# Performance work log

Hardware: AMD Instinct MI355X
Metric: run time of the kernel (lower is better)

## Reference

```python
import jax, jax.numpy as jnp
import numpy as np

B, T, C = 2, 2048, 1024
H = 16
D = C // H  # 64
SCALE = 1.0 / np.sqrt(D)


def setup_inputs() -> dict:
    key = jax.random.key(0)
    k1, k2, k3 = jax.random.split(key, 3)
    x = jax.random.normal(k1, (B, T, C), dtype=jnp.float32)
    Wqkv = jax.random.normal(k2, (C, 3 * C), dtype=jnp.float32) * 0.02
    bqkv = jnp.zeros((3 * C,), dtype=jnp.float32)
    Wo = jax.random.normal(k3, (C, C), dtype=jnp.float32) * 0.02
    bo = jnp.zeros((C,), dtype=jnp.float32)
    return {"x": x, "Wqkv": Wqkv, "bqkv": bqkv, "Wo": Wo, "bo": bo}


def reference(x, Wqkv, bqkv, Wo, bo):
    Bsz, Tlen, Cdim = x.shape
    qkv = x @ Wqkv + bqkv                       # [B,T,3C]
    qkv = qkv.reshape(Bsz, Tlen, 3, H, D)
    qkv = jnp.transpose(qkv, (2, 0, 3, 1, 4))   # [3,B,H,T,D]
    q, k, v = qkv[0], qkv[1], qkv[2]
    att = jnp.einsum("bhqd,bhkd->bhqk", q, k) * SCALE
    # NOTE: faithful to source: mask keeps positions where k >= q
    i = jnp.arange(Tlen)
    mask = i[None, :] >= i[:, None]             # [T,T], entry [q,k]: k >= q
    att = jnp.where(mask[None, None], att, -jnp.inf)
    att = jax.nn.softmax(att, axis=-1)
    # dropout p=0.0 (inference) -> identity
    y = jnp.einsum("bhqk,bhkd->bhqd", att, v)   # [B,H,T,D]
    y = jnp.transpose(y, (0, 2, 1, 3)).reshape(Bsz, Tlen, Cdim)
    y = y @ Wo + bo
    return y
```

## Files before the change

kernel.cpp:

```cpp
#include <hip/hip_runtime.h>
#include <hip/hip_bf16.h>
#include <cstdint>
#include <cstddef>

typedef __bf16 bf16_t;
typedef __bf16 bf16x8 __attribute__((ext_vector_type(8)));
typedef __bf16 bf16x4 __attribute__((ext_vector_type(4)));
typedef short short4v __attribute__((ext_vector_type(4)));
typedef float f32x4 __attribute__((ext_vector_type(4)));

#define NB 2
#define NT 2048
#define NC 1024
#define NH 16
#define ND 64
#define NM (NB * NT)
#define N3 (3 * NC)
#define QSCALE_LOG2E 0.18033688011112042f

#define GLOAD_LDS16(gptr, lptr)                                                          \
  __builtin_amdgcn_global_load_lds((const __attribute__((address_space(1))) void*)(gptr), \
                                   (__attribute__((address_space(3))) void*)(lptr), 16, 0, 0)

__global__ __launch_bounds__(256) void cast_f32_bf16_k(const float* __restrict__ in,
                                                       bf16_t* __restrict__ out, int n) {
  int i = (blockIdx.x * 256 + threadIdx.x) * 4;
  if (i + 3 < n) {
    const float4 v = *(const float4*)(in + i);
    bf16x4 o;
    o[0] = (bf16_t)v.x; o[1] = (bf16_t)v.y; o[2] = (bf16_t)v.z; o[3] = (bf16_t)v.w;
    *(bf16x4*)(out + i) = o;
  }
}

__global__ __launch_bounds__(256) void transpose_cast_k(const float* __restrict__ in,
                                                        bf16_t* __restrict__ out,
                                                        int R, int Ccols) {
  __shared__ float tile[32][33];
  int tc = blockIdx.x * 32;
  int tr = blockIdx.y * 32;
  int lx = threadIdx.x & 31;
  int ly = threadIdx.x >> 5;
#pragma unroll
  for (int i = 0; i < 32; i += 8)
    tile[ly + i][lx] = in[(size_t)(tr + ly + i) * Ccols + tc + lx];
  __syncthreads();
#pragma unroll
  for (int i = 0; i < 32; i += 8)
    out[(size_t)(tc + ly + i) * R + tr + lx] = (bf16_t)tile[lx][ly + i];
}

template <int K>
__device__ __forceinline__ void gemm_mainloop(const bf16_t* __restrict__ A,
                                              const bf16_t* __restrict__ Bt,
                                              int m0, int n0, f32x4 acc[4][4],
                                              bf16_t* lds) {
  bf16_t* As = lds;
  bf16_t* Bs = lds + 4096;
  const int tid = threadIdx.x;
  const int lane = tid & 63;
  const int w = tid >> 6;
  const int wm = (w & 1) * 64;
  const int wn = (w >> 1) * 64;
  const int quad = lane >> 4;
  const int l16 = lane & 15;

  for (int k0 = 0; k0 < K; k0 += 32) {
#pragma unroll
    for (int i = 0; i < 2; ++i) {
      const int gb = w * 128 + i * 64;
      const int g = gb + lane;
      GLOAD_LDS16(A + (size_t)(m0 + (g >> 2)) * K + k0 + (g & 3) * 8, As + gb * 8);
      GLOAD_LDS16(Bt + (size_t)(n0 + (g >> 2)) * K + k0 + (g & 3) * 8, Bs + gb * 8);
    }
    __syncthreads();
    bf16x8 af[4], bfr[4];
#pragma unroll
    for (int i = 0; i < 4; ++i)
      af[i] = *(const bf16x8*)(As + (wm + i * 16 + l16) * 32 + quad * 8);
#pragma unroll
    for (int j = 0; j < 4; ++j)
      bfr[j] = *(const bf16x8*)(Bs + (wn + j * 16 + l16) * 32 + quad * 8);
#pragma unroll
    for (int i = 0; i < 4; ++i)
#pragma unroll
      for (int j = 0; j < 4; ++j)
        acc[i][j] = __builtin_amdgcn_mfma_f32_16x16x32_bf16(af[i], bfr[j], acc[i][j], 0, 0, 0);
    __syncthreads();
  }
}

__global__ __launch_bounds__(256) void qkv_gemm_k(const bf16_t* __restrict__ A,
                                                  const bf16_t* __restrict__ Bt,
                                                  const float* __restrict__ bias,
                                                  bf16_t* __restrict__ qb,
                                                  bf16_t* __restrict__ kb,
                                                  bf16_t* __restrict__ vb) {
  __shared__ __align__(16) bf16_t lds[8192];
  const int m0 = blockIdx.y * 128, n0 = blockIdx.x * 128;
  f32x4 acc[4][4] = {};
  gemm_mainloop<NC>(A, Bt, m0, n0, acc, lds);

  const int lane = threadIdx.x & 63;
  const int w = threadIdx.x >> 6;
  const int wm = (w & 1) * 64, wn = (w >> 1) * 64;
  const int quad = lane >> 4, l16 = lane & 15;
#pragma unroll
  for (int i = 0; i < 4; ++i)
#pragma unroll
    for (int j = 0; j < 4; ++j) {
      const int n = n0 + wn + j * 16 + l16;
      const float bn = bias[n];
      const int which = n >> 10;
      const int rem = n & 1023;
      const int h = rem >> 6, d = rem & 63;
      bf16_t* dst = (which == 0) ? qb : (which == 1) ? kb : vb;
      const float sc = (which == 0) ? QSCALE_LOG2E : 1.0f;
#pragma unroll
      for (int r = 0; r < 4; ++r) {
        const int m = m0 + wm + i * 16 + quad * 4 + r;
        const int b = m >> 11, t = m & 2047;
        const size_t bh = (size_t)b * NH + h;
        dst[(bh * NT + t) * ND + d] = (bf16_t)((acc[i][j][r] + bn) * sc);
      }
    }
}

__global__ __launch_bounds__(256) void vtile_k(const bf16_t* __restrict__ v,
                                               bf16_t* __restrict__ vt2) {
  const int bh = blockIdx.x >> 5, c = blockIdx.x & 31;
  const bf16_t* src = v + ((size_t)bh * NT + c * 64) * ND;
  bf16_t* dst = vt2 + ((size_t)bh * 32 + c) * 4096;
#pragma unroll
  for (int it = 0; it < 4; ++it) {
    const int slot = it * 256 + threadIdx.x;
    const int g = slot >> 6, d = slot & 63;
    bf16x4 val;
#pragma unroll
    for (int j = 0; j < 4; ++j) val[j] = src[(size_t)(g * 4 + j) * ND + d];
    *(bf16x4*)(dst + (size_t)slot * 4) = val;
  }
}

__global__ __launch_bounds__(256, 4) void attn_k(const bf16_t* __restrict__ q,
                                                 const bf16_t* __restrict__ k,
                                                 const bf16_t* __restrict__ vt2,
                                                 bf16_t* __restrict__ y ) {
  const int bh = blockIdx.x & 31;
  const int u = (blockIdx.x >> 5) & 7;
  const int r4 = blockIdx.x >> 8;
  const int T = r4 * 8 + ((r4 & 1) ? (7 - u) : u);
  const int b = bh >> 4, h = bh & 15;

  const bf16_t* qp = q + (size_t)bh * NT * ND;
  const bf16_t* kp = k + (size_t)bh * NT * ND;
  const bf16_t* vp = vt2 + (size_t)bh * 32 * 4096;

  __shared__ __align__(16) bf16_t kbuf[2][4096];
  __shared__ __align__(16) bf16_t vbuf[2][4096];

  const int lane = threadIdx.x & 63;
  const int w = threadIdx.x >> 6;
  const int quad = lane >> 4, l16 = lane & 15;
  const int qv = T * 64 + w * 16 + l16;

  const bf16x8 qf0 = *(const bf16x8*)(qp + (size_t)qv * ND + quad * 8);
  const bf16x8 qf1 = *(const bf16x8*)(qp + (size_t)qv * ND + 32 + quad * 8);

  float m = -INFINITY, l = 0.f;
  f32x4 o[4];
#pragma unroll
  for (int dj = 0; dj < 4; ++dj) o[dj] = (f32x4){0.f, 0.f, 0.f, 0.f};

  auto stage = [&](int c, int bi) {
    const bf16_t* kc = kp + (size_t)c * 64 * ND;
    const bf16_t* vc = vp + (size_t)c * 4096;
#pragma unroll
    for (int i = 0; i < 2; ++i) {
      const int gb = w * 128 + i * 64;
      const int s = gb + lane;
      const int row = s >> 3;
      const int cs = (s & 7) ^ (row & 7);
      GLOAD_LDS16(kc + ((size_t)row * 8 + cs) * 8, kbuf[bi] + gb * 8);
      GLOAD_LDS16(vc + (size_t)s * 8, vbuf[bi] + gb * 8);
    }
  };

  stage(T, 0);
  int cur = 0;
  for (int c = T; c < 32; ++c) {
    __syncthreads();
    if (c + 1 < 32) stage(c + 1, cur ^ 1);

    const bf16_t* kt = kbuf[cur];
    const bf16_t* vt = vbuf[cur];
    const int t0 = c * 64;

    f32x4 sv[4];
#pragma unroll
    for (int kj = 0; kj < 4; ++kj) {
      const int kr = kj * 16 + l16;
      const int sw = kr & 7;
      const bf16x8 a0 = *(const bf16x8*)(kt + ((size_t)kr * 8 + (quad ^ sw)) * 8);
      const bf16x8 a1 = *(const bf16x8*)(kt + ((size_t)kr * 8 + ((4 + quad) ^ sw)) * 8);
      f32x4 z = {0.f, 0.f, 0.f, 0.f};
      z = __builtin_amdgcn_mfma_f32_16x16x32_bf16(a0, qf0, z, 0, 0, 0);
      z = __builtin_amdgcn_mfma_f32_16x16x32_bf16(a1, qf1, z, 0, 0, 0);
      sv[kj] = z;
    }
    if (c == T) {
#pragma unroll
      for (int kj = 0; kj < 4; ++kj)
#pragma unroll
        for (int r = 0; r < 4; ++r)
          if (t0 + kj * 16 + quad * 4 + r < qv) sv[kj][r] = -INFINITY;
    }
    float mx = -INFINITY;
#pragma unroll
    for (int kj = 0; kj < 4; ++kj)
#pragma unroll
      for (int r = 0; r < 4; ++r) mx = fmaxf(mx, sv[kj][r]);
    mx = fmaxf(mx, __shfl_xor(mx, 16));
    mx = fmaxf(mx, __shfl_xor(mx, 32));
    const float mnew = fmaxf(m, mx);
    const float alpha = exp2f(m - mnew);
    m = mnew;
    float rs = 0.f;
#pragma unroll
    for (int kj = 0; kj < 4; ++kj)
#pragma unroll
      for (int r = 0; r < 4; ++r) {
        const float p = exp2f(sv[kj][r] - mnew);
        sv[kj][r] = p;
        rs += p;
      }
    rs += __shfl_xor(rs, 16);
    rs += __shfl_xor(rs, 32);
    l = l * alpha + rs;
    short4v pf[4];
#pragma unroll
    for (int kj = 0; kj < 4; ++kj) {
      bf16x4 pb;
#pragma unroll
      for (int r = 0; r < 4; ++r) pb[r] = (bf16_t)sv[kj][r];
      pf[kj] = __builtin_bit_cast(short4v, pb);
    }
#pragma unroll
    for (int dj = 0; dj < 4; ++dj) {
      o[dj][0] *= alpha; o[dj][1] *= alpha; o[dj][2] *= alpha; o[dj][3] *= alpha;
#pragma unroll
      for (int kj = 0; kj < 4; ++kj) {
        const bf16x4 a =
            *(const bf16x4*)(vt + ((size_t)(kj * 4 + quad) * 64 + dj * 16 + l16) * 4);
        o[dj] = __builtin_amdgcn_mfma_f32_16x16x16bf16_1k(
            __builtin_bit_cast(short4v, a), pf[kj], o[dj], 0, 0, 0);
      }
    }
    cur ^= 1;
  }

  const float inv = 1.0f / l;
  const size_t base = ((size_t)b * NT + qv) * NC + h * 64;
#pragma unroll
  for (int dj = 0; dj < 4; ++dj) {
    bf16x4 va;
#pragma unroll
    for (int r = 0; r < 4; ++r) va[r] = (bf16_t)(o[dj][r] * inv);
    *(bf16x4*)(y + base + dj * 16 + quad * 4) = va;
  }
}

__global__ __launch_bounds__(256) void out_gemm_k(const bf16_t* __restrict__ A,
                                                  const bf16_t* __restrict__ Bt,
                                                  const float* __restrict__ bias,
                                                  float* __restrict__ out) {
  __shared__ __align__(16) bf16_t lds[8192];
  const int m0 = blockIdx.y * 128, n0 = blockIdx.x * 128;
  f32x4 acc[4][4] = {};
  gemm_mainloop<NC>(A, Bt, m0, n0, acc, lds);

  const int lane = threadIdx.x & 63;
  const int w = threadIdx.x >> 6;
  const int wm = (w & 1) * 64, wn = (w >> 1) * 64;
  const int quad = lane >> 4, l16 = lane & 15;
#pragma unroll
  for (int i = 0; i < 4; ++i)
#pragma unroll
    for (int j = 0; j < 4; ++j) {
      const int n = n0 + wn + j * 16 + l16;
      const float bn = bias[n];
#pragma unroll
      for (int r = 0; r < 4; ++r) {
        const int m = m0 + wm + i * 16 + quad * 4 + r;
        out[(size_t)m * NC + n] = acc[i][j][r] + bn;
      }
    }
}

extern "C" void kernel_launch(void* const* d_in, const int* in_sizes, int n_in,
                              void* d_out, int out_size, void* d_ws, size_t ws_size,
                              hipStream_t stream) {
  const float* x = (const float*)d_in[0];
  const float* Wqkv = (const float*)d_in[1];
  const float* bqkv = (const float*)d_in[2];
  const float* Wo = (const float*)d_in[3];
  const float* bo = (const float*)d_in[4];
  float* out = (float*)d_out;

  char* p = (char*)d_ws;
  bf16_t* xbf = (bf16_t*)p;   p += (size_t)NM * NC * sizeof(bf16_t);
  bf16_t* wqkvT = (bf16_t*)p; p += (size_t)N3 * NC * sizeof(bf16_t);
  bf16_t* woT = (bf16_t*)p;   p += (size_t)NC * NC * sizeof(bf16_t);
  bf16_t* qb = (bf16_t*)p;    p += (size_t)NB * NH * NT * ND * sizeof(bf16_t);
  bf16_t* kb = (bf16_t*)p;    p += (size_t)NB * NH * NT * ND * sizeof(bf16_t);
  bf16_t* vb = (bf16_t*)p;    p += (size_t)NB * NH * NT * ND * sizeof(bf16_t);
  bf16_t* yb = (bf16_t*)p;    p += (size_t)NM * NC * sizeof(bf16_t);
  bf16_t* vt2 = xbf;

  hipLaunchKernelGGL(cast_f32_bf16_k, dim3(NM * NC / 1024), dim3(256), 0, stream,
                     x, xbf, NM * NC);
  hipLaunchKernelGGL(transpose_cast_k, dim3(N3 / 32, NC / 32), dim3(256), 0, stream,
                     Wqkv, wqkvT, NC, N3);
  hipLaunchKernelGGL(transpose_cast_k, dim3(NC / 32, NC / 32), dim3(256), 0, stream,
                     Wo, woT, NC, NC);
  hipLaunchKernelGGL(qkv_gemm_k, dim3(N3 / 128, NM / 128), dim3(256), 0, stream,
                     xbf, wqkvT, bqkv, qb, kb, vb);
  hipLaunchKernelGGL(vtile_k, dim3(32 * 32), dim3(256), 0, stream, vb, vt2);
  hipLaunchKernelGGL(attn_k, dim3(1024), dim3(256), 0, stream, qb, kb, vt2, yb);
  hipLaunchKernelGGL(out_gemm_k, dim3(NC / 128, NM / 128), dim3(256), 0, stream,
                     yb, woT, bo, out);
}
```

Baseline: 194.6 us.

## Fuse prep kernels, write V tiled from QKV GEMM, MFMA rowsum in attention

The x cast and both weight transpose-casts are merged into one prep launch. The QKV GEMM epilogue now writes V directly in the tiled layout attention expects, which removes the separate vtile kernel and its extra pass over memory. In attention, the softmax row sum is computed with an MFMA against a ones vector from the bf16-rounded probabilities instead of a scalar reduction with shuffles. The rescale of the output accumulator is skipped when no lane's max changed. Together these aim to cut launch overhead, memory traffic and VALU work. The cost is a warp-wide vote per tile and a row sum taken from bf16-rounded values.

```diff
diff --git a/kernel.cpp b/kernel.cpp
--- a/kernel.cpp
+++ b/kernel.cpp
@@ -22,32 +22,39 @@
   __builtin_amdgcn_global_load_lds((const __attribute__((address_space(1))) void*)(gptr), \
                                    (__attribute__((address_space(3))) void*)(lptr), 16, 0, 0)
 
-__global__ __launch_bounds__(256) void cast_f32_bf16_k(const float* __restrict__ in,
-                                                       bf16_t* __restrict__ out, int n) {
-  int i = (blockIdx.x * 256 + threadIdx.x) * 4;
-  if (i + 3 < n) {
-    const float4 v = *(const float4*)(in + i);
+__global__ __launch_bounds__(256) void prep_k(const float* __restrict__ x,
+                                              const float* __restrict__ Wqkv,
+                                              const float* __restrict__ Wo,
+                                              bf16_t* __restrict__ xbf,
+                                              bf16_t* __restrict__ wqkvT,
+                                              bf16_t* __restrict__ woT) {
+  __shared__ float tile[32][33];
+  const int bx = blockIdx.x;
+  if (bx < 4096) {
+    const int i = (bx * 256 + threadIdx.x) * 4;
+    const float4 v = *(const float4*)(x + i);
     bf16x4 o;
     o[0] = (bf16_t)v.x; o[1] = (bf16_t)v.y; o[2] = (bf16_t)v.z; o[3] = (bf16_t)v.w;
-    *(bf16x4*)(out + i) = o;
+    *(bf16x4*)(xbf + i) = o;
+    return;
   }
-}
-
-__global__ __launch_bounds__(256) void transpose_cast_k(const float* __restrict__ in,
-                                                        bf16_t* __restrict__ out,
-                                                        int R, int Ccols) {
-  __shared__ float tile[32][33];
-  int tc = blockIdx.x * 32;
-  int tr = blockIdx.y * 32;
-  int lx = threadIdx.x & 31;
-  int ly = threadIdx.x >> 5;
+  const int t = bx - 4096;
+  const int cxi = t & 127;
+  const int tr = (t >> 7) * 32;
+  const float* in;
+  bf16_t* out;
+  int Ccols, tc;
+  if (cxi < 96) { in = Wqkv; out = wqkvT; Ccols = 3072; tc = cxi * 32; }
+  else          { in = Wo;   out = woT;   Ccols = 1024; tc = (cxi - 96) * 32; }
+  const int lx = threadIdx.x & 31;
+  const int ly = threadIdx.x >> 5;
 #pragma unroll
   for (int i = 0; i < 32; i += 8)
     tile[ly + i][lx] = in[(size_t)(tr + ly + i) * Ccols + tc + lx];
   __syncthreads();
 #pragma unroll
   for (int i = 0; i < 32; i += 8)
-    out[(size_t)(tc + ly + i) * R + tr + lx] = (bf16_t)tile[lx][ly + i];
+    out[(size_t)(tc + ly + i) * 1024 + tr + lx] = (bf16_t)tile[lx][ly + i];
 }
 
 template <int K>
@@ -95,7 +102,7 @@
                                                   const float* __restrict__ bias,
                                                   bf16_t* __restrict__ qb,
                                                   bf16_t* __restrict__ kb,
-                                                  bf16_t* __restrict__ vb) {
+                                                  bf16_t* __restrict__ vt2) {
   __shared__ __align__(16) bf16_t lds[8192];
   const int m0 = blockIdx.y * 128, n0 = blockIdx.x * 128;
   f32x4 acc[4][4] = {};
@@ -114,32 +121,23 @@
       const int which = n >> 10;
       const int rem = n & 1023;
       const int h = rem >> 6, d = rem & 63;
-      bf16_t* dst = (which == 0) ? qb : (which == 1) ? kb : vb;
-      const float sc = (which == 0) ? QSCALE_LOG2E : 1.0f;
-#pragma unroll
-      for (int r = 0; r < 4; ++r) {
-        const int m = m0 + wm + i * 16 + quad * 4 + r;
-        const int b = m >> 11, t = m & 2047;
-        const size_t bh = (size_t)b * NH + h;
-        dst[(bh * NT + t) * ND + d] = (bf16_t)((acc[i][j][r] + bn) * sc);
+      const int mb = m0 + wm + i * 16 + quad * 4;
+      const int b = mb >> 11, t4 = mb & 2047;
+      const size_t bh = (size_t)b * NH + h;
+      if (which == 2) {
+        const int c = t4 >> 6, g = (t4 >> 2) & 15;
+        bf16x4 val;
+#pragma unroll
+        for (int r = 0; r < 4; ++r) val[r] = (bf16_t)(acc[i][j][r] + bn);
+        *(bf16x4*)(vt2 + ((bh * 32 + c) * 1024 + (size_t)g * 64 + d) * 4) = val;
+      } else {
+        bf16_t* dst = (which == 0) ? qb : kb;
+        const float sc = (which == 0) ? QSCALE_LOG2E : 1.0f;
+#pragma unroll
+        for (int r = 0; r < 4; ++r)
+          dst[(bh * NT + t4 + r) * ND + d] = (bf16_t)((acc[i][j][r] + bn) * sc);
       }
     }
-}
-
-__global__ __launch_bounds__(256) void vtile_k(const bf16_t* __restrict__ v,
-                                               bf16_t* __restrict__ vt2) {
-  const int bh = blockIdx.x >> 5, c = blockIdx.x & 31;
-  const bf16_t* src = v + ((size_t)bh * NT + c * 64) * ND;
-  bf16_t* dst = vt2 + ((size_t)bh * 32 + c) * 4096;
-#pragma unroll
-  for (int it = 0; it < 4; ++it) {
-    const int slot = it * 256 + threadIdx.x;
-    const int g = slot >> 6, d = slot & 63;
-    bf16x4 val;
-#pragma unroll
-    for (int j = 0; j < 4; ++j) val[j] = src[(size_t)(g * 4 + j) * ND + d];
-    *(bf16x4*)(dst + (size_t)slot * 4) = val;
-  }
 }
 
 __global__ __launch_bounds__(256, 4) void attn_k(const bf16_t* __restrict__ q,
@@ -167,6 +165,8 @@
   const bf16x8 qf0 = *(const bf16x8*)(qp + (size_t)qv * ND + quad * 8);
   const bf16x8 qf1 = *(const bf16x8*)(qp + (size_t)qv * ND + 32 + quad * 8);
 
+  const short4v ones = {0x3F80, 0x3F80, 0x3F80, 0x3F80};
+
   float m = -INFINITY, l = 0.f;
   f32x4 o[4];
 #pragma unroll
@@ -215,39 +215,37 @@
         for (int r = 0; r < 4; ++r)
           if (t0 + kj * 16 + quad * 4 + r < qv) sv[kj][r] = -INFINITY;
     }
-    float mx = -INFINITY;
-#pragma unroll
-    for (int kj = 0; kj < 4; ++kj)
-#pragma unroll
-      for (int r = 0; r < 4; ++r) mx = fmaxf(mx, sv[kj][r]);
+    float mx = fmaxf(fmaxf(sv[0][0], sv[0][1]), fmaxf(sv[0][2], sv[0][3]));
+#pragma unroll
+    for (int kj = 1; kj < 4; ++kj)
+      mx = fmaxf(mx, fmaxf(fmaxf(sv[kj][0], sv[kj][1]), fmaxf(sv[kj][2], sv[kj][3])));
     mx = fmaxf(mx, __shfl_xor(mx, 16));
     mx = fmaxf(mx, __shfl_xor(mx, 32));
     const float mnew = fmaxf(m, mx);
     const float alpha = exp2f(m - mnew);
     m = mnew;
-    float rs = 0.f;
-#pragma unroll
-    for (int kj = 0; kj < 4; ++kj)
-#pragma unroll
-      for (int r = 0; r < 4; ++r) {
-        const float p = exp2f(sv[kj][r] - mnew);
-        sv[kj][r] = p;
-        rs += p;
-      }
-    rs += __shfl_xor(rs, 16);
-    rs += __shfl_xor(rs, 32);
-    l = l * alpha + rs;
     short4v pf[4];
 #pragma unroll
     for (int kj = 0; kj < 4; ++kj) {
       bf16x4 pb;
 #pragma unroll
-      for (int r = 0; r < 4; ++r) pb[r] = (bf16_t)sv[kj][r];
+      for (int r = 0; r < 4; ++r) pb[r] = (bf16_t)exp2f(sv[kj][r] - mnew);
       pf[kj] = __builtin_bit_cast(short4v, pb);
     }
+    f32x4 zs = {0.f, 0.f, 0.f, 0.f};
+#pragma unroll
+    for (int kj = 0; kj < 4; ++kj)
+      zs = __builtin_amdgcn_mfma_f32_16x16x16bf16_1k(ones, pf[kj], zs, 0, 0, 0);
+    const bool resc = __any(alpha != 1.0f);
+    l = resc ? (l * alpha + zs[0]) : (l + zs[0]);
+    if (resc) {
+#pragma unroll
+      for (int dj = 0; dj < 4; ++dj) {
+        o[dj][0] *= alpha; o[dj][1] *= alpha; o[dj][2] *= alpha; o[dj][3] *= alpha;
+      }
+    }
 #pragma unroll
     for (int dj = 0; dj < 4; ++dj) {
-      o[dj][0] *= alpha; o[dj][1] *= alpha; o[dj][2] *= alpha; o[dj][3] *= alpha;
 #pragma unroll
       for (int kj = 0; kj < 4; ++kj) {
         const bf16x4 a =
@@ -313,19 +311,13 @@
   bf16_t* woT = (bf16_t*)p;   p += (size_t)NC * NC * sizeof(bf16_t);
   bf16_t* qb = (bf16_t*)p;    p += (size_t)NB * NH * NT * ND * sizeof(bf16_t);
   bf16_t* kb = (bf16_t*)p;    p += (size_t)NB * NH * NT * ND * sizeof(bf16_t);
-  bf16_t* vb = (bf16_t*)p;    p += (size_t)NB * NH * NT * ND * sizeof(bf16_t);
+  bf16_t* vt2 = (bf16_t*)p;   p += (size_t)NB * NH * NT * ND * sizeof(bf16_t);
   bf16_t* yb = (bf16_t*)p;    p += (size_t)NM * NC * sizeof(bf16_t);
-  bf16_t* vt2 = xbf;
-
-  hipLaunchKernelGGL(cast_f32_bf16_k, dim3(NM * NC / 1024), dim3(256), 0, stream,
-                     x, xbf, NM * NC);
-  hipLaunchKernelGGL(transpose_cast_k, dim3(N3 / 32, NC / 32), dim3(256), 0, stream,
-                     Wqkv, wqkvT, NC, N3);
-  hipLaunchKernelGGL(transpose_cast_k, dim3(NC / 32, NC / 32), dim3(256), 0, stream,
-                     Wo, woT, NC, NC);
+
+  hipLaunchKernelGGL(prep_k, dim3(8192), dim3(256), 0, stream,
+                     x, Wqkv, Wo, xbf, wqkvT, woT);
   hipLaunchKernelGGL(qkv_gemm_k, dim3(N3 / 128, NM / 128), dim3(256), 0, stream,
-                     xbf, wqkvT, bqkv, qb, kb, vb);
-  hipLaunchKernelGGL(vtile_k, dim3(32 * 32), dim3(256), 0, stream, vb, vt2);
+                     xbf, wqkvT, bqkv, qb, kb, vt2);
   hipLaunchKernelGGL(attn_k, dim3(1024), dim3(256), 0, stream, qb, kb, vt2, yb);
   hipLaunchKernelGGL(out_gemm_k, dim3(NC / 128, NM / 128), dim3(256), 0, stream,
                      yb, woT, bo, out);
```

New measurement: 181.8 us. 1.07x faster.
